# Kernel optimization log

Measured on AMD Instinct MI355X. Metric: run time of the kernel, lower is better.

## Reference

```python
import jax, jax.numpy as jnp
import numpy as np

B, T_IN, D = 16, 2048, 384
OUT_LEN = 4096  # == max over batch of sum(repeat_count), enforced in setup_inputs


def setup_inputs() -> dict:
    key = jax.random.key(0)
    kx, kr = jax.random.split(key)
    x = jax.random.normal(kx, (B, T_IN, D), dtype=jnp.float32)
    r = jax.random.randint(kr, (B, T_IN), 0, 4, dtype=jnp.int32)
    # cap each row's cumulative sum at OUT_LEN, then force row 0 to hit OUT_LEN
    # exactly so that int(max(sum(repeat_count))) == OUT_LEN (static shape).
    c = jnp.minimum(jnp.cumsum(r, axis=-1), OUT_LEN)
    r = jnp.diff(c, prepend=0, axis=-1)
    r = r.at[0, -1].add(OUT_LEN - c[0, -1])
    return {"x": x, "repeat_count": r.astype(jnp.int32),
            "output_max_seq_len": OUT_LEN}


def reference(x, repeat_count, output_max_seq_len):
    # Torch module builds a one-hot expansion matrix M [B, T_out, T_in] and does
    # bmm(M, x). Equivalently: output frame p of batch b copies input token j
    # where j = searchsorted(cumsum(repeat_count[b]), p, side='right'),
    # and frames p >= sum(repeat_count[b]) are zero (rows of M left as zeros).
    cum = jnp.cumsum(repeat_count, axis=-1)          # [B, T_in]
    output_seq_len = cum[:, -1]                      # [B]
    pos = jnp.arange(output_max_seq_len)             # [T_out]
    # per-batch gather indices  [B, T_out]
    idx = jax.vmap(lambda c: jnp.searchsorted(c, pos, side='right'))(cum)
    idx = jnp.clip(idx, 0, x.shape[1] - 1)
    out = jnp.take_along_axis(x, idx[..., None], axis=1)  # [B, T_out, D]
    valid = (pos[None, :] < output_seq_len[:, None])       # [B, T_out]
    out = out * valid[:, :, None].astype(x.dtype)
    return out, output_seq_len
```

## Files before the change

### kernel.cpp

```cpp
#include <hip/hip_runtime.h>

#define NB      16
#define T_IN    2048
#define OUT_LEN 4096
#define D       384
#define D4      (D / 4)

__global__ __launch_bounds__(256) void cumsum_kernel(const int* __restrict__ r,
                                                     int* __restrict__ cum,
                                                     float* __restrict__ seqlen_out) {
    const int b   = blockIdx.x;
    const int tid = threadIdx.x;
    const int4* rb = (const int4*)(r + b * T_IN);
    int4*       cb = (int4*)(cum + b * T_IN);

    int4 v0 = rb[tid * 2];
    int4 v1 = rb[tid * 2 + 1];
    int v[8] = {v0.x, v0.y, v0.z, v0.w, v1.x, v1.y, v1.z, v1.w};

    int s = 0;
#pragma unroll
    for (int i = 0; i < 8; ++i) { s += v[i]; v[i] = s; }

    const int lane = tid & 63;
    const int wid  = tid >> 6;
    int pre = s;
#pragma unroll
    for (int off = 1; off < 64; off <<= 1) {
        int up = __shfl_up(pre, off, 64);
        if (lane >= off) pre += up;
    }

    __shared__ int wsum[4];
    if (lane == 63) wsum[wid] = pre;
    __syncthreads();

    int excl = pre - s;
    for (int w = 0; w < wid; ++w) excl += wsum[w];

#pragma unroll
    for (int i = 0; i < 8; ++i) v[i] += excl;

    cb[tid * 2]     = make_int4(v[0], v[1], v[2], v[3]);
    cb[tid * 2 + 1] = make_int4(v[4], v[5], v[6], v[7]);

    if (tid == 255) seqlen_out[b] = (float)v[7];
}

__global__ __launch_bounds__(256) void search_kernel(const int* __restrict__ cum,
                                                     int* __restrict__ idx) {
    const int g = blockIdx.x * 256 + threadIdx.x;
    if (g >= NB * OUT_LEN) return;
    const int b = g >> 12;
    const int t = g & (OUT_LEN - 1);
    const int* cb = cum + b * T_IN;
    const int seq = cb[T_IN - 1];

    int res = -1;
    if (t < seq) {
        int lo = 0, hi = T_IN;
        while (lo < hi) {
            int mid = (lo + hi) >> 1;
            if (cb[mid] <= t) lo = mid + 1; else hi = mid;
        }
        res = lo < (T_IN - 1) ? lo : (T_IN - 1);
    }
    idx[g] = res;
}

__global__ __launch_bounds__(256) void gather_kernel(const float4* __restrict__ x,
                                                     const int* __restrict__ idx,
                                                     float4* __restrict__ out) {
    const unsigned row0  = blockIdx.x * 8u;
    const unsigned base  = row0 * D4;
    const unsigned b     = row0 >> 12;
    const float4*  xb    = x + (size_t)b * T_IN * D4;

#pragma unroll
    for (int k = 0; k < 3; ++k) {
        const unsigned local = threadIdx.x + k * 256u;
        const unsigned rloc  = local / D4;
        const unsigned d     = local - rloc * D4;
        const int irow = idx[row0 + rloc];
        float4 val = make_float4(0.f, 0.f, 0.f, 0.f);
        if (irow >= 0) val = xb[(unsigned)irow * D4 + d];
        out[base + local] = val;
    }
}

extern "C" void kernel_launch(void* const* d_in, const int* in_sizes, int n_in,
                              void* d_out, int out_size, void* d_ws, size_t ws_size,
                              hipStream_t stream) {
    const float* x  = (const float*)d_in[0];
    const int*   rc = (const int*)d_in[1];

    float* out        = (float*)d_out;
    float* seqlen_out = out + (size_t)NB * OUT_LEN * D;

    int* cum = (int*)d_ws;
    int* idx = cum + NB * T_IN;

    cumsum_kernel<<<NB, 256, 0, stream>>>(rc, cum, seqlen_out);

    const int n_pos = NB * OUT_LEN;
    search_kernel<<<n_pos / 256, 256, 0, stream>>>(cum, idx);

    const unsigned n_rows = (unsigned)NB * OUT_LEN;
    gather_kernel<<<n_rows / 8, 256, 0, stream>>>((const float4*)x, idx,
                                                  (float4*)out);
}
```

Baseline: 147.6 us.

## Fuse binary search into gather kernel and use nontemporal output stores

Removes the separate search kernel and its idx buffer round-trip. Each gather block now has 8 threads binary-search the cumsum for its 8 output rows, share the indices through LDS, and then copy the rows. Output writes become nontemporal stores so the write-once output stream does less cache pollution. In exchange, each block adds a serial binary-search latency and a barrier before any gather load can issue.

New measurement: 158.0 us. +7.0%, slower.

```diff
diff --git a/kernel.cpp b/kernel.cpp
--- a/kernel.cpp
+++ b/kernel.cpp
@@ -5,6 +5,8 @@
 #define OUT_LEN 4096
 #define D       384
 #define D4      (D / 4)
+
+typedef float f32x4 __attribute__((ext_vector_type(4)));
 
 __global__ __launch_bounds__(256) void cumsum_kernel(const int* __restrict__ r,
                                                      int* __restrict__ cum,
@@ -47,44 +49,42 @@
     if (tid == 255) seqlen_out[b] = (float)v[7];
 }
 
-__global__ __launch_bounds__(256) void search_kernel(const int* __restrict__ cum,
-                                                     int* __restrict__ idx) {
-    const int g = blockIdx.x * 256 + threadIdx.x;
-    if (g >= NB * OUT_LEN) return;
-    const int b = g >> 12;
-    const int t = g & (OUT_LEN - 1);
+__global__ __launch_bounds__(256) void regulate_kernel(const f32x4* __restrict__ x,
+                                                       const int* __restrict__ cum,
+                                                       f32x4* __restrict__ out) {
+    const unsigned row0 = blockIdx.x * 8u;
+    const unsigned b    = row0 >> 12;
     const int* cb = cum + b * T_IN;
-    const int seq = cb[T_IN - 1];
 
-    int res = -1;
-    if (t < seq) {
-        int lo = 0, hi = T_IN;
-        while (lo < hi) {
-            int mid = (lo + hi) >> 1;
-            if (cb[mid] <= t) lo = mid + 1; else hi = mid;
+    __shared__ int sidx[8];
+    if (threadIdx.x < 8) {
+        const int t   = (int)(row0 & (OUT_LEN - 1)) + (int)threadIdx.x;
+        const int seq = cb[T_IN - 1];
+        int res = -1;
+        if (t < seq) {
+            int lo = 0, hi = T_IN;
+            while (lo < hi) {
+                int mid = (lo + hi) >> 1;
+                if (cb[mid] <= t) lo = mid + 1; else hi = mid;
+            }
+            res = lo < (T_IN - 1) ? lo : (T_IN - 1);
         }
-        res = lo < (T_IN - 1) ? lo : (T_IN - 1);
+        sidx[threadIdx.x] = res;
     }
-    idx[g] = res;
-}
+    __syncthreads();
 
-__global__ __launch_bounds__(256) void gather_kernel(const float4* __restrict__ x,
-                                                     const int* __restrict__ idx,
-                                                     float4* __restrict__ out) {
-    const unsigned row0  = blockIdx.x * 8u;
-    const unsigned base  = row0 * D4;
-    const unsigned b     = row0 >> 12;
-    const float4*  xb    = x + (size_t)b * T_IN * D4;
+    const f32x4*  xb   = x + (size_t)b * T_IN * D4;
+    const unsigned base = row0 * (unsigned)D4;
 
 #pragma unroll
     for (int k = 0; k < 3; ++k) {
         const unsigned local = threadIdx.x + k * 256u;
         const unsigned rloc  = local / D4;
         const unsigned d     = local - rloc * D4;
-        const int irow = idx[row0 + rloc];
-        float4 val = make_float4(0.f, 0.f, 0.f, 0.f);
+        const int irow = sidx[rloc];
+        f32x4 val = (f32x4)(0.f);
         if (irow >= 0) val = xb[(unsigned)irow * D4 + d];
-        out[base + local] = val;
+        __builtin_nontemporal_store(val, &out[base + local]);
     }
 }
 
@@ -98,14 +98,10 @@
     float* seqlen_out = out + (size_t)NB * OUT_LEN * D;
 
     int* cum = (int*)d_ws;
-    int* idx = cum + NB * T_IN;
 
     cumsum_kernel<<<NB, 256, 0, stream>>>(rc, cum, seqlen_out);
 
-    const int n_pos = NB * OUT_LEN;
-    search_kernel<<<n_pos / 256, 256, 0, stream>>>(cum, idx);
-
     const unsigned n_rows = (unsigned)NB * OUT_LEN;
-    gather_kernel<<<n_rows / 8, 256, 0, stream>>>((const float4*)x, idx,
-                                                  (float4*)out);
+    regulate_kernel<<<n_rows / 8, 256, 0, stream>>>((const f32x4*)x, cum,
+                                                    (f32x4*)out);
 }
```
